# Performance work log

Hardware: AMD Instinct MI355X
Metric: run time of the kernel (lower is better)

The kernel has to match this reference:

```python
import jax, jax.numpy as jnp
import numpy as np

N = 100000        # nodes
E = 1600000       # edges (N * avg_degree 16)
D_IN = 128
D_OUT = 32
OBS_T = 60        # observation_time -> decay table size 60*OBS_T = 3600
T_MAX = 60 * OBS_T


def setup_inputs() -> dict:
    key = jax.random.key(0)
    ks = jax.random.split(key, 8)
    inp = {
        "input": jax.random.normal(ks[0], (N, D_IN), dtype=jnp.float32),
        "W": jax.random.normal(ks[1], (D_IN, D_OUT), dtype=jnp.float32) * (np.sqrt(2.0) / np.sqrt(D_IN)),
        # decay weights are abs(normal(0, 0.02)) in the original; rand*0.04 is same scale
        "decay_weight1": jnp.abs(jax.random.normal(ks[2], (T_MAX, 1), dtype=jnp.float32) * 0.02),
        "decay_weight2": jnp.abs(jax.random.normal(ks[3], (T_MAX, 1), dtype=jnp.float32) * 0.02),
        "edge_row": jax.random.randint(ks[4], (E,), 0, N, dtype=jnp.int32),
        "edge_col": jax.random.randint(ks[5], (E,), 0, N, dtype=jnp.int32),
        # zero-based interval index; equals (adj_value - 1) of the original code
        "edge_time": jax.random.randint(ks[6], (E,), 0, T_MAX, dtype=jnp.int32),
        "arrive_time": jax.random.randint(ks[7], (N,), 0, T_MAX, dtype=jnp.int32),
        "observation_time": OBS_T,
    }
    return inp


def reference(input, W, decay_weight1, decay_weight2,
              edge_row, edge_col, edge_time, arrive_time, observation_time):
    n_nodes = input.shape[0]
    # h = relu(input @ W)  [N, D_OUT]
    h = jax.nn.relu(jnp.matmul(input, W))
    # one-hot(interval) @ decay_weight1 == embedding lookup  -> per-edge decay scalar
    decay = decay_weight1[edge_time, 0]                        # [E]
    # SpecialSpmm: out[i] = sum_{edges (i,j)} decay_e * h[j]  (gather-scale-scatter)
    msgs = decay[:, None] * h[edge_col]                        # [E, D_OUT]
    h_prime = jax.ops.segment_sum(msgs, edge_row, num_segments=n_nodes)
    # outlayer window decay: one-hot(60*T - arrive - 1) @ decay_weight2 == lookup
    win_idx = 60 * observation_time - arrive_time - 1          # [N] in [0, 60*T)
    h_prime = decay_weight2[win_idx, 0][:, None] * h_prime
    return h_prime
```

## Files before the change

kernel.cpp:

```cpp
#include <hip/hip_runtime.h>

#define N_NODES 100000
#define N_EDGES 1600000
#define D_IN    128
#define D_OUT   32
#define CROWS   2048
#define NCB     49
#define NSH     8
#define CAP_A   4500
#define DEPTH   48
#define NROWP   (NCB * CROWS)
#define CBCAP   36864
#define CAPW    768
#define RPB3    32
#define K3_BLKS (NCB * 64)
#define GEMM_BLKS ((N_NODES + 63) / 64)
#define GRID_A  2048
#define EPB_A   ((N_EDGES + GRID_A - 1) / GRID_A)

typedef __attribute__((ext_vector_type(8))) short bf16x8;
typedef __attribute__((ext_vector_type(4))) float f32x4;

__device__ inline short f2bf(float f) {
    union { float f; unsigned u; } v; v.f = f;
    unsigned r = (v.u + 0x7FFFu + ((v.u >> 16) & 1u)) >> 16;
    return (short)r;
}

union SMemGA {
    struct { short wbt[D_IN * D_OUT]; } g;
    struct { uint2 lbin[NCB][DEPTH]; int lcnt[NCB]; int gbase[NCB]; } a;
};

__global__ __launch_bounds__(256) void gemm_phaseA_kernel(
    const float* __restrict__ input, const float* __restrict__ W,
    const int* __restrict__ erow,    const int* __restrict__ ecol,
    const int* __restrict__ etime,
    unsigned short* __restrict__ h16,
    int* __restrict__ gcur,
    uint2* __restrict__ segA)
{
    __shared__ SMemGA sm;
    const int tid = threadIdx.x;

    if (blockIdx.x < GEMM_BLKS) {
        for (int i = tid; i < D_IN * D_OUT; i += 256) {
            const int k = i >> 5, c = i & 31;
            sm.g.wbt[c * D_IN + k] = f2bf(W[i]);
        }
        __syncthreads();

        const int wave = tid >> 6;
        const int lane = tid & 63;
        const int r0   = blockIdx.x * 64 + wave * 16;
        const int c16  = lane & 15;
        const int quad = lane >> 4;

        int ra = r0 + c16;
        if (ra >= N_NODES) ra = N_NODES - 1;
        const float* arow = input + (size_t)ra * D_IN;

        f32x4 acc0 = {0.f, 0.f, 0.f, 0.f};
        f32x4 acc1 = {0.f, 0.f, 0.f, 0.f};
#pragma unroll
        for (int q = 0; q < 4; ++q) {
            const float* ap = arow + q * 32 + quad * 8;
            f32x4 a0 = *(const f32x4*)(ap);
            f32x4 a1 = *(const f32x4*)(ap + 4);
            bf16x8 af;
            af[0] = f2bf(a0.x); af[1] = f2bf(a0.y); af[2] = f2bf(a0.z); af[3] = f2bf(a0.w);
            af[4] = f2bf(a1.x); af[5] = f2bf(a1.y); af[6] = f2bf(a1.z); af[7] = f2bf(a1.w);
            bf16x8 b0 = *(const bf16x8*)(sm.g.wbt + (c16)      * D_IN + q * 32 + quad * 8);
            bf16x8 b1 = *(const bf16x8*)(sm.g.wbt + (c16 + 16) * D_IN + q * 32 + quad * 8);
            acc0 = __builtin_amdgcn_mfma_f32_16x16x32_bf16(af, b0, acc0, 0, 0, 0);
            acc1 = __builtin_amdgcn_mfma_f32_16x16x32_bf16(af, b1, acc1, 0, 0, 0);
        }
#pragma unroll
        for (int i = 0; i < 4; ++i) {
            const int rr = r0 + quad * 4 + i;
            if (rr < N_NODES) {
                h16[(size_t)rr * D_OUT + c16]      = (unsigned short)f2bf(fmaxf(acc0[i], 0.f));
                h16[(size_t)rr * D_OUT + c16 + 16] = (unsigned short)f2bf(fmaxf(acc1[i], 0.f));
            }
        }
    } else {
        const int blk   = blockIdx.x - GEMM_BLKS;
        const int shard = blk & (NSH - 1);
        const int wv    = tid >> 6;
        const int ln    = tid & 63;

        if (tid < NCB) sm.a.lcnt[tid] = 0;
        __syncthreads();

        const int e_beg = blk * EPB_A;
        const int e_end = min(e_beg + EPB_A, N_EDGES);

        for (int e = e_beg + tid; e < e_end; e += 256) {
            const int row = erow[e];
            const int cb  = row >> 11;
            uint2 p;
            p.x = (unsigned)ecol[e] | ((unsigned)(row & (CROWS - 1)) << 17);
            p.y = (unsigned)etime[e];
            const int pos = atomicAdd(&sm.a.lcnt[cb], 1);
            if (pos < DEPTH) sm.a.lbin[cb][pos] = p;
            else {
                const int gp = atomicAdd(&gcur[(cb * NSH + shard) * 16], 1);
                if (gp < CAP_A) segA[(size_t)(cb * NSH + shard) * CAP_A + gp] = p;
            }
        }
        __syncthreads();

        if (tid < NCB) {
            const int c = min(sm.a.lcnt[tid], DEPTH);
            sm.a.gbase[tid] = atomicAdd(&gcur[(tid * NSH + shard) * 16], c);
        }
        __syncthreads();

        for (int bin = wv; bin < NCB; bin += 4) {
            const int c  = min(sm.a.lcnt[bin], DEPTH);
            const int gb = sm.a.gbase[bin];
            uint2* seg = segA + (size_t)(bin * NSH + shard) * CAP_A;
            for (int k = ln; k < c; k += 64)
                if (gb + k < CAP_A) seg[gb + k] = sm.a.lbin[bin][k];
        }
    }
}

__global__ __launch_bounds__(512) void sortcb_kernel(
    const int* __restrict__ gcur, const uint2* __restrict__ segA,
    int* __restrict__ rstart, int* __restrict__ fcur,
    unsigned* __restrict__ spk2)
{
    __shared__ int hist[CROWS];
    __shared__ int sstart[CROWS];
    __shared__ int curs[CROWS];
    __shared__ int part[512];
    __shared__ int snsh[NSH];

    const int tid = threadIdx.x;
    const int cb  = blockIdx.x;

    if (tid < NSH) snsh[tid] = min(gcur[(cb * NSH + tid) * 16], CAP_A);
    for (int t = tid; t < CROWS; t += 512) hist[t] = 0;
    __syncthreads();

    for (int s = 0; s < NSH; ++s) {
        const int n = snsh[s];
        const uint2* seg = segA + (size_t)(cb * NSH + s) * CAP_A;
        for (int i = tid; i < n; i += 512)
            atomicAdd(&hist[(seg[i].x >> 17) & (CROWS - 1)], 1);
    }
    __syncthreads();

    int tmp[4]; int s0 = 0;
    const int base = tid * 4;
#pragma unroll
    for (int k = 0; k < 4; ++k) { tmp[k] = hist[base + k]; s0 += tmp[k]; }
    part[tid] = s0;
    __syncthreads();
    for (int off = 1; off < 512; off <<= 1) {
        int v = part[tid];
        if (tid >= off) v += part[tid - off];
        __syncthreads(); part[tid] = v; __syncthreads();
    }
    int run = part[tid] - s0;
#pragma unroll
    for (int k = 0; k < 4; ++k) { sstart[base + k] = run; curs[base + k] = run; run += tmp[k]; }
    __syncthreads();

    for (int t = tid; t < CROWS; t += 512) {
        rstart[cb * CROWS + t] = cb * CBCAP + sstart[t];
        fcur[cb * CROWS + t]   = hist[t];
    }

    unsigned* dst = spk2 + (size_t)cb * CBCAP;
    for (int s = 0; s < NSH; ++s) {
        const int n = snsh[s];
        const uint2* seg = segA + (size_t)(cb * NSH + s) * CAP_A;
        for (int i = tid; i < n; i += 512) {
            const uint2 p  = seg[i];
            const int   rl = (p.x >> 17) & (CROWS - 1);
            const unsigned rec = (p.x & 0x1FFFFu) | (p.y << 20);
            dst[atomicAdd(&curs[rl], 1)] = rec;
        }
    }
}

__global__ __launch_bounds__(256) void row_reduce_kernel(
    const unsigned short* __restrict__ h16, const int* __restrict__ rstart,
    const int* __restrict__ fcur, const unsigned* __restrict__ spk2,
    const float* __restrict__ dw1, const float* __restrict__ dw2,
    const int* __restrict__ arrive, const int* __restrict__ obs,
    float* __restrict__ out)
{
    __shared__ unsigned st[CAPW];
    __shared__ int ls[RPB3];
    __shared__ int lc[RPB3];

    const int b  = blockIdx.x;
    const int cb = b >> 6;
    const int r0 = cb * CROWS + (b & 63) * RPB3;
    if (r0 >= N_NODES) return;
    const int tid = threadIdx.x;

    if (tid < RPB3) {
        ls[tid] = rstart[r0 + tid];
        lc[tid] = fcur[r0 + tid];
    }
    __syncthreads();

    const int sbeg  = ls[0];
    const int span  = ls[RPB3 - 1] + lc[RPB3 - 1] - sbeg;
    const int spanc = min(span, CAPW);
    for (int i = tid; i < spanc; i += 256) st[i] = spk2[(size_t)sbeg + i];
    __syncthreads();

    const int g  = tid >> 3;
    const int li = tid & 7;
    const int row = r0 + g;
    const int beg = ls[g] - sbeg;
    const int n   = lc[g];
    const unsigned* recs = (beg + n <= CAPW)
        ? (const unsigned*)&st[beg]
        : (const unsigned*)&spk2[(size_t)sbeg + beg];
    const unsigned short* hp = h16 + li * 4;

    float a0 = 0.f, a1 = 0.f, a2 = 0.f, a3 = 0.f;
    int j = 0;
    for (; j + 8 <= n; j += 8) {
#pragma unroll
        for (int u = 0; u < 8; ++u) {
            const unsigned rec = recs[j + u];
            const uint2 hv = *(const uint2*)(hp + ((size_t)(rec & 0x1FFFFu) << 5));
            const float w  = dw1[rec >> 20];
            a0 = fmaf(w, __uint_as_float(hv.x << 16),         a0);
            a1 = fmaf(w, __uint_as_float(hv.x & 0xFFFF0000u), a1);
            a2 = fmaf(w, __uint_as_float(hv.y << 16),         a2);
            a3 = fmaf(w, __uint_as_float(hv.y & 0xFFFF0000u), a3);
        }
    }
    for (; j < n; ++j) {
        const unsigned rec = recs[j];
        const uint2 hv = *(const uint2*)(hp + ((size_t)(rec & 0x1FFFFu) << 5));
        const float w  = dw1[rec >> 20];
        a0 = fmaf(w, __uint_as_float(hv.x << 16),         a0);
        a1 = fmaf(w, __uint_as_float(hv.x & 0xFFFF0000u), a1);
        a2 = fmaf(w, __uint_as_float(hv.y << 16),         a2);
        a3 = fmaf(w, __uint_as_float(hv.y & 0xFFFF0000u), a3);
    }

    const int T = 60 * obs[0];
    const float sdw = dw2[T - arrive[row] - 1];
    float4 o;
    o.x = a0 * sdw; o.y = a1 * sdw; o.z = a2 * sdw; o.w = a3 * sdw;
    *(float4*)(out + ((size_t)row << 5) + li * 4) = o;
}

extern "C" void kernel_launch(void* const* d_in, const int* in_sizes, int n_in,
                              void* d_out, int out_size, void* d_ws, size_t ws_size,
                              hipStream_t stream)
{
    const float* input  = (const float*)d_in[0];
    const float* W      = (const float*)d_in[1];
    const float* dw1    = (const float*)d_in[2];
    const float* dw2    = (const float*)d_in[3];
    const int*   erow   = (const int*)d_in[4];
    const int*   ecol   = (const int*)d_in[5];
    const int*   etime  = (const int*)d_in[6];
    const int*   arrive = (const int*)d_in[7];
    const int*   obs    = (const int*)d_in[8];

    float* out = (float*)d_out;

    char* p = (char*)d_ws;
    unsigned short* h16 = (unsigned short*)p;
    p += (size_t)N_NODES * D_OUT * 2;
    p = (char*)(((size_t)p + 255) & ~(size_t)255);
    int* gcur = (int*)p;
    p += (size_t)NCB * NSH * 16 * 4;
    int* rstart = (int*)p;
    p += (size_t)NROWP * 4;
    int* fcur = (int*)p;
    p += (size_t)NROWP * 4;
    p = (char*)(((size_t)p + 255) & ~(size_t)255);
    uint2* segA = (uint2*)p;
    p += (size_t)NCB * NSH * CAP_A * 8;
    p = (char*)(((size_t)p + 255) & ~(size_t)255);
    unsigned* spk2 = (unsigned*)p;

    hipMemsetAsync(gcur, 0, (size_t)NCB * NSH * 16 * 4, stream);

    gemm_phaseA_kernel<<<GEMM_BLKS + GRID_A, 256, 0, stream>>>(
        input, W, erow, ecol, etime, h16, gcur, segA);
    sortcb_kernel<<<NCB, 512, 0, stream>>>(gcur, segA, rstart, fcur, spk2);
    row_reduce_kernel<<<K3_BLKS, 256, 0, stream>>>(
        h16, rstart, fcur, spk2, dw1, dw2, arrive, obs, out);
}
```

Measured before the change: 203.2 us.

## Split per-chunk counting sort into per-shard histogram and placement kernels

The single 49-block sort kernel becomes two kernels running 392 blocks, one per (chunk, shard) segment. The first builds a per-shard row histogram in global memory. The second sums the shard histograms, computes row starts plus a per-shard prefix offset, and scatters its shard's edges directly. This raises GPU occupancy well beyond 49 workgroups on a device with many CUs, at the cost of an extra kernel launch, histogram round-trips through global memory, and each placement block rereading eight histograms.

Result: no change. 201.9 us (-0.6%).

```diff
diff --git a/kernel.cpp b/kernel.cpp
--- a/kernel.cpp
+++ b/kernel.cpp
@@ -7,6 +7,7 @@
 #define CROWS   2048
 #define NCB     49
 #define NSH     8
+#define NSEG    (NCB * NSH)
 #define CAP_A   4500
 #define DEPTH   48
 #define NROWP   (NCB * CROWS)
@@ -126,63 +127,88 @@
     }
 }
 
-__global__ __launch_bounds__(512) void sortcb_kernel(
+__global__ __launch_bounds__(256) void hist392_kernel(
     const int* __restrict__ gcur, const uint2* __restrict__ segA,
+    int* __restrict__ hshard)
+{
+    __shared__ int hist[CROWS];
+    const int b   = blockIdx.x;
+    const int tid = threadIdx.x;
+    const int n   = min(gcur[b * 16], CAP_A);
+    const uint2* seg = segA + (size_t)b * CAP_A;
+
+    for (int t = tid; t < CROWS; t += 256) hist[t] = 0;
+    __syncthreads();
+    for (int i = tid; i < n; i += 256)
+        atomicAdd(&hist[(seg[i].x >> 17) & (CROWS - 1)], 1);
+    __syncthreads();
+    int* hb = hshard + (size_t)b * CROWS;
+    for (int t = tid; t < CROWS; t += 256) hb[t] = hist[t];
+}
+
+__global__ __launch_bounds__(256) void place392_kernel(
+    const int* __restrict__ gcur, const uint2* __restrict__ segA,
+    const int* __restrict__ hshard,
     int* __restrict__ rstart, int* __restrict__ fcur,
     unsigned* __restrict__ spk2)
 {
-    __shared__ int hist[CROWS];
+    __shared__ int tot[CROWS];
+    __shared__ int pre[CROWS];
+    __shared__ int curs[CROWS];
     __shared__ int sstart[CROWS];
-    __shared__ int curs[CROWS];
-    __shared__ int part[512];
-    __shared__ int snsh[NSH];
-
+    __shared__ int part[256];
+
+    const int b   = blockIdx.x;
+    const int cb  = b >> 3;
+    const int s   = b & 7;
     const int tid = threadIdx.x;
-    const int cb  = blockIdx.x;
-
-    if (tid < NSH) snsh[tid] = min(gcur[(cb * NSH + tid) * 16], CAP_A);
-    for (int t = tid; t < CROWS; t += 512) hist[t] = 0;
-    __syncthreads();
-
-    for (int s = 0; s < NSH; ++s) {
-        const int n = snsh[s];
-        const uint2* seg = segA + (size_t)(cb * NSH + s) * CAP_A;
-        for (int i = tid; i < n; i += 512)
-            atomicAdd(&hist[(seg[i].x >> 17) & (CROWS - 1)], 1);
-    }
-    __syncthreads();
-
-    int tmp[4]; int s0 = 0;
-    const int base = tid * 4;
-#pragma unroll
-    for (int k = 0; k < 4; ++k) { tmp[k] = hist[base + k]; s0 += tmp[k]; }
+
+    for (int r = tid; r < CROWS; r += 256) { tot[r] = 0; pre[r] = 0; }
+    __syncthreads();
+    for (int sp = 0; sp < NSH; ++sp) {
+        const int* hs = hshard + (size_t)(cb * NSH + sp) * CROWS;
+        for (int r = tid; r < CROWS; r += 256) {
+            const int v = hs[r];
+            tot[r] += v;
+            if (sp < s) pre[r] += v;
+        }
+    }
+    __syncthreads();
+
+    int tmp[8]; int s0 = 0;
+    const int base = tid * 8;
+#pragma unroll
+    for (int k = 0; k < 8; ++k) { tmp[k] = tot[base + k]; s0 += tmp[k]; }
     part[tid] = s0;
     __syncthreads();
-    for (int off = 1; off < 512; off <<= 1) {
+    for (int off = 1; off < 256; off <<= 1) {
         int v = part[tid];
         if (tid >= off) v += part[tid - off];
         __syncthreads(); part[tid] = v; __syncthreads();
     }
     int run = part[tid] - s0;
 #pragma unroll
-    for (int k = 0; k < 4; ++k) { sstart[base + k] = run; curs[base + k] = run; run += tmp[k]; }
-    __syncthreads();
-
-    for (int t = tid; t < CROWS; t += 512) {
-        rstart[cb * CROWS + t] = cb * CBCAP + sstart[t];
-        fcur[cb * CROWS + t]   = hist[t];
-    }
-
+    for (int k = 0; k < 8; ++k) {
+        sstart[base + k] = run;
+        curs[base + k]   = run + pre[base + k];
+        run += tmp[k];
+    }
+    __syncthreads();
+
+    if (s == 0) {
+        for (int r = tid; r < CROWS; r += 256) {
+            rstart[cb * CROWS + r] = cb * CBCAP + sstart[r];
+            fcur[cb * CROWS + r]   = tot[r];
+        }
+    }
+
+    const int n = min(gcur[b * 16], CAP_A);
+    const uint2* seg = segA + (size_t)b * CAP_A;
     unsigned* dst = spk2 + (size_t)cb * CBCAP;
-    for (int s = 0; s < NSH; ++s) {
-        const int n = snsh[s];
-        const uint2* seg = segA + (size_t)(cb * NSH + s) * CAP_A;
-        for (int i = tid; i < n; i += 512) {
-            const uint2 p  = seg[i];
-            const int   rl = (p.x >> 17) & (CROWS - 1);
-            const unsigned rec = (p.x & 0x1FFFFu) | (p.y << 20);
-            dst[atomicAdd(&curs[rl], 1)] = rec;
-        }
+    for (int i = tid; i < n; i += 256) {
+        const uint2 p  = seg[i];
+        const int   rl = (p.x >> 17) & (CROWS - 1);
+        dst[atomicAdd(&curs[rl], 1)] = (p.x & 0x1FFFFu) | (p.y << 20);
     }
 }
 
@@ -277,22 +303,27 @@
     p += (size_t)N_NODES * D_OUT * 2;
     p = (char*)(((size_t)p + 255) & ~(size_t)255);
     int* gcur = (int*)p;
-    p += (size_t)NCB * NSH * 16 * 4;
+    p += (size_t)NSEG * 16 * 4;
     int* rstart = (int*)p;
     p += (size_t)NROWP * 4;
     int* fcur = (int*)p;
     p += (size_t)NROWP * 4;
     p = (char*)(((size_t)p + 255) & ~(size_t)255);
+    int* hshard = (int*)p;
+    p += (size_t)NSEG * CROWS * 4;
+    p = (char*)(((size_t)p + 255) & ~(size_t)255);
     uint2* segA = (uint2*)p;
-    p += (size_t)NCB * NSH * CAP_A * 8;
+    p += (size_t)NSEG * CAP_A * 8;
     p = (char*)(((size_t)p + 255) & ~(size_t)255);
     unsigned* spk2 = (unsigned*)p;
 
-    hipMemsetAsync(gcur, 0, (size_t)NCB * NSH * 16 * 4, stream);
+    hipMemsetAsync(gcur, 0, (size_t)NSEG * 16 * 4, stream);
 
     gemm_phaseA_kernel<<<GEMM_BLKS + GRID_A, 256, 0, stream>>>(
         input, W, erow, ecol, etime, h16, gcur, segA);
-    sortcb_kernel<<<NCB, 512, 0, stream>>>(gcur, segA, rstart, fcur, spk2);
+    hist392_kernel<<<NSEG, 256, 0, stream>>>(gcur, segA, hshard);
+    place392_kernel<<<NSEG, 256, 0, stream>>>(
+        gcur, segA, hshard, rstart, fcur, spk2);
     row_reduce_kernel<<<K3_BLKS, 256, 0, stream>>>(
         h16, rstart, fcur, spk2, dw1, dw2, arrive, obs, out);
 }
```
